# Optimization experiments

Measured on AMD Instinct MI355X. Metric: run time of the kernel, lower is better.

Reference implementation:

```python
import jax, jax.numpy as jnp
import numpy as np

N = 512          # num_atoms (sqrt of number of pairwise edges)
H = 512          # h_nf / in_edge_nf
T_STEPS = 100    # recon.total_time
K_RANK = 3       # coord_dims / low-rank k
POWER_STEPS = 10


def setup_inputs() -> dict:
    key = jax.random.key(0)
    ks = jax.random.split(key, 6)
    s = 1.0 / np.sqrt(H)
    return {
        "gnn_edge_out": jax.random.normal(ks[0], (N * N, H), jnp.float32),
        "W1": jax.random.normal(ks[1], (H, H), jnp.float32) * s,   # edge_mlp1 Linear
        "b1": jnp.zeros((H,), jnp.float32),
        "W2": jax.random.normal(ks[2], (H, 2), jnp.float32) * s,    # edge_mlp2 Linear(h_nf, edge_out_nf=2)
        "b2": jnp.zeros((2,), jnp.float32),
        "noise_x": jax.random.normal(ks[3], (N, K_RANK), jnp.float32),  # randn added to low-rank init
        "u_init": jax.random.normal(ks[4], (N, K_RANK), jnp.float32),   # power-iteration random starts
    }


def reference(gnn_edge_out, W1, b1, W2, b2, noise_x, u_init):
    # ---- DistWeightLayer ----
    h = jax.nn.relu(gnn_edge_out @ W1 + b1)          # edge_mlp1 (MLP, 1 layer)
    emb = jnp.sum(h)[None]                           # sum over dims (0,1), unsqueeze -> (1,)
    e = jax.nn.softplus(h @ W2 + b2)                 # (N*N, 2) softplus(edge_mlp2)
    D_init = e[:, 0].reshape(N, N) * (1.0 - jnp.eye(N, dtype=e.dtype))
    W = e[:, 1].reshape(N, N)

    # ---- dist_to_gram ----
    D = D_init
    D_row = jnp.mean(D, axis=0)                      # (N,)
    D_col = jnp.mean(D, axis=1, keepdims=True)       # (N,1)
    D_mean = jnp.mean(D)
    B = -0.5 * (D - D_row - D_col + D_mean)

    # ---- low_rank_approx_power (k=3, deflation) ----
    A_lr = B
    us = []
    for i in range(K_RANK):
        u = u_init[:, i:i + 1]                       # (N,1)
        for _ in range(POWER_STEPS):
            u = u / jnp.maximum(jnp.linalg.norm(u), 1e-3)  # F.normalize eps=0.001
            u = A_lr @ u
        eig_sq = jnp.sum(u * u)
        u = u * (eig_sq + 0.01) ** 0.25              # u / pow(eig_sq+0.01, -0.25)
        us.append(u)
        A_lr = A_lr - u @ u.T
    X = jnp.concatenate(us, axis=1) + noise_x        # (N,3)

    # ---- 100-step distance-geometry descent (step_func) ----
    def U_fn(Xc):
        diff = Xc[:, None, :] - Xc[None, :, :]       # (N,N,3)
        Dx = jnp.sqrt(jnp.sum(diff * diff, axis=-1) + 0.01)  # tsg_eps
        return jnp.sum(W * jnp.square(D_init - Dx))

    def step(Xc, t):
        g = jax.grad(U_fn)(Xc)
        dX = -0.1 * g                                # tsg_eps1
        speed = jnp.sqrt(jnp.sum(dX * dX, axis=-1, keepdims=True) + 0.001)  # tsg_eps2
        alpha_t = 0.1 + (5.0 - 0.1) * (T_STEPS - t) / T_STEPS
        scale = alpha_t * jnp.tanh(speed / alpha_t) / speed
        return Xc + dX * scale, None

    X_pred, _ = jax.lax.scan(step, X, jnp.arange(T_STEPS, dtype=X.dtype))
    return (D_init, W, emb, X_pred)
```

## Files before the change

kernel.cpp:

```cpp
#include <hip/hip_runtime.h>
#include <hip/hip_bf16.h>
#include <math.h>

#define NN 512
#define ROWS (NN * NN)
#define HH 512

#define NB 16
#define NT 512
#define RPB 32

#define WS_EMB   0
#define WS_COLP  4096
#define WS_U0    (WS_COLP + 32*512)
#define WS_U1    (WS_U0 + 512)
#define WS_X0    (WS_U1 + 512)
#define WS_X1    (WS_X0 + 2048)
#define WS_W1T   (WS_X1 + 2048)
#define WS_BAR   (WS_W1T + 131072)

typedef __attribute__((ext_vector_type(8))) short bf16x8;
typedef __attribute__((ext_vector_type(4))) float f32x4;

#define AGENT __HIP_MEMORY_SCOPE_AGENT

__device__ __forceinline__ short f2bf(float f) {
    union { float f; unsigned u; } v; v.f = f;
    unsigned r = v.u + 0x7fffu + ((v.u >> 16) & 1u);
    return (short)(r >> 16);
}

__device__ __forceinline__ unsigned pack_bf2(float lo, float hi) {
    return __builtin_amdgcn_perm(__float_as_uint(hi), __float_as_uint(lo),
                                 0x07060302u);
}

__device__ __forceinline__ float softplus_f(float x) {
    return fmaxf(x, 0.0f) + log1pf(expf(-fabsf(x)));
}

__device__ __forceinline__ unsigned long long pk64(float a, float b) {
    return ((unsigned long long)__float_as_uint(b) << 32) |
           (unsigned long long)__float_as_uint(a);
}

__global__ void w1t_prep(const float* __restrict__ W1, short* __restrict__ W1T)
{
    __shared__ float tile[32][33];
    const int bx = blockIdx.x & 15;
    const int by = blockIdx.x >> 4;
    const int tx = threadIdx.x & 31;
    const int ty = threadIdx.x >> 5;
    const int n0 = bx * 32, k0 = by * 32;
    #pragma unroll
    for (int i = 0; i < 4; i++)
        tile[ty + i * 8][tx] = W1[(size_t)(k0 + ty + i * 8) * HH + n0 + tx];
    __syncthreads();
    #pragma unroll
    for (int i = 0; i < 4; i++)
        W1T[(size_t)(n0 + ty + i * 8) * HH + k0 + tx] = f2bf(tile[tx][ty + i * 8]);
}

__global__ __launch_bounds__(512, 4) void fused_mlp(
    const float* __restrict__ A, const short* __restrict__ W1T,
    const float* __restrict__ b1, const float* __restrict__ W2,
    const float* __restrict__ b2, float* __restrict__ outD,
    float* __restrict__ outW, float* __restrict__ embpart)
{
    __shared__ short As[2][64 * 72];
    __shared__ float sp0[8][64], sp1[8][64];
    __shared__ float semb[8];

    const int tid = threadIdx.x;
    const int lane = tid & 63;
    const int wc = tid >> 6;
    const int l15 = lane & 15;
    const int l4 = lane >> 4;
    const int row0 = blockIdx.x * 64;

    f32x4 acc[4][4];
    #pragma unroll
    for (int m = 0; m < 4; m++)
        #pragma unroll
        for (int n = 0; n < 4; n++) {
            f32x4 z = {0.0f, 0.0f, 0.0f, 0.0f};
            acc[m][n] = z;
        }

    const int sr = tid >> 3;
    const int sk8 = (tid & 7) * 8;
    const float* agp = A + (size_t)(row0 + sr) * HH + sk8;

    {
        float4 a0 = *(const float4*)agp;
        float4 a1 = *(const float4*)(agp + 4);
        uint4 w = {pack_bf2(a0.x, a0.y), pack_bf2(a0.z, a0.w),
                   pack_bf2(a1.x, a1.y), pack_bf2(a1.z, a1.w)};
        *(uint4*)&As[0][sr * 72 + sk8] = w;
    }
    __syncthreads();

    int cur = 0;
    #pragma unroll 1
    for (int s = 0; s < 8; s++) {
        const int k0 = s * 64;
        float4 pv0, pv1;
        if (s < 7) {
            pv0 = *(const float4*)(agp + k0 + 64);
            pv1 = *(const float4*)(agp + k0 + 68);
        }
        for (int kc = 0; kc < 2; kc++) {
            const int kb = k0 + kc * 32;
            bf16x8 bfr[4], af[4];
            #pragma unroll
            for (int n = 0; n < 4; n++) {
                int col = wc * 64 + n * 16 + l15;
                bfr[n] = *(const bf16x8*)(W1T + (size_t)col * HH + kb + l4 * 8);
            }
            #pragma unroll
            for (int m = 0; m < 4; m++)
                af[m] = *(const bf16x8*)&As[cur][(m * 16 + l15) * 72 + kc * 32 + l4 * 8];
            #pragma unroll
            for (int m = 0; m < 4; m++)
                #pragma unroll
                for (int n = 0; n < 4; n++)
                    acc[m][n] = __builtin_amdgcn_mfma_f32_16x16x32_bf16(
                        af[m], bfr[n], acc[m][n], 0, 0, 0);
        }
        if (s < 7) {
            uint4 w = {pack_bf2(pv0.x, pv0.y), pack_bf2(pv0.z, pv0.w),
                       pack_bf2(pv1.x, pv1.y), pack_bf2(pv1.z, pv1.w)};
            *(uint4*)&As[cur ^ 1][sr * 72 + sk8] = w;
        }
        __syncthreads();
        cur ^= 1;
    }

    float b1c[4], w20[4], w21[4];
    #pragma unroll
    for (int n = 0; n < 4; n++) {
        int col = wc * 64 + n * 16 + l15;
        b1c[n] = b1[col];
        w20[n] = W2[col * 2 + 0];
        w21[n] = W2[col * 2 + 1];
    }
    float embl = 0.0f;
    #pragma unroll
    for (int m = 0; m < 4; m++) {
        #pragma unroll
        for (int j = 0; j < 4; j++) {
            float s0 = 0.0f, s1 = 0.0f;
            #pragma unroll
            for (int n = 0; n < 4; n++) {
                float h = fmaxf(acc[m][n][j] + b1c[n], 0.0f);
                s0 = fmaf(h, w20[n], s0);
                s1 = fmaf(h, w21[n], s1);
                embl += h;
            }
            #pragma unroll
            for (int st = 1; st < 16; st <<= 1) {
                s0 += __shfl_xor(s0, st);
                s1 += __shfl_xor(s1, st);
            }
            if (l15 == 0) {
                int row = m * 16 + l4 * 4 + j;
                sp0[wc][row] = s0;
                sp1[wc][row] = s1;
            }
        }
    }
    #pragma unroll
    for (int st = 1; st < 64; st <<= 1) embl += __shfl_xor(embl, st);
    if (lane == 0) semb[wc] = embl;
    __syncthreads();
    if (tid < 64) {
        int gr = row0 + tid;
        float p0 = b2[0], p1 = b2[1];
        #pragma unroll
        for (int w = 0; w < 8; w++) { p0 += sp0[w][tid]; p1 += sp1[w][tid]; }
        int di = gr >> 9, dj = gr & 511;
        outD[gr] = (di == dj) ? 0.0f : softplus_f(p0);
        outW[gr] = softplus_f(p1);
    }
    if (tid == 0) {
        float e = 0.0f;
        #pragma unroll
        for (int w = 0; w < 8; w++) e += semb[w];
        embpart[blockIdx.x] = e;
    }
}

__device__ __forceinline__ void gbar(int* cnt, int target)
{
    __syncthreads();
    if (threadIdx.x == 0)
        __hip_atomic_fetch_add(cnt, 1, __ATOMIC_RELAXED, AGENT);
    if (threadIdx.x < 64) {
        while (__hip_atomic_load(cnt, __ATOMIC_RELAXED, AGENT) < target)
            __builtin_amdgcn_s_sleep(1);
    }
    __syncthreads();
}

__device__ __forceinline__ void block_sum5(float* v, float (*red)[8], int tid) {
    #pragma unroll
    for (int s = 1; s < 64; s <<= 1)
        #pragma unroll
        for (int q = 0; q < 5; q++) v[q] += __shfl_xor(v[q], s);
    if ((tid & 63) == 0)
        #pragma unroll
        for (int q = 0; q < 5; q++) red[q][tid >> 6] = v[q];
    __syncthreads();
    #pragma unroll
    for (int q = 0; q < 5; q++) {
        float r = 0.0f;
        #pragma unroll
        for (int i = 0; i < 8; i++) r += red[q][i];
        v[q] = r;
    }
    __syncthreads();
}

__device__ __forceinline__ float block_sum1(float v, float (*red)[8], int tid) {
    #pragma unroll
    for (int s = 1; s < 64; s <<= 1) v += __shfl_xor(v, s);
    if ((tid & 63) == 0) red[0][tid >> 6] = v;
    __syncthreads();
    float r = 0.0f;
    #pragma unroll
    for (int i = 0; i < 8; i++) r += red[0][i];
    __syncthreads();
    return r;
}

__global__ __launch_bounds__(512, 1) void coop_post(
    const float* __restrict__ Dg, const float* __restrict__ Wg,
    const float* __restrict__ noise, const float* __restrict__ uinit,
    float* __restrict__ outE, float* __restrict__ outX,
    float* __restrict__ ws)
{
    __shared__ float Dl[RPB][516];
    __shared__ float S1[RPB][516];
    __shared__ float Xl[512][4];
    __shared__ float ul[512];
    __shared__ float upl[3][512];
    __shared__ float cm[512];
    __shared__ float rm[RPB];
    __shared__ float red5[5][8];

    const int tid = threadIdx.x;
    const int bid = blockIdx.x;
    const int r0 = bid * RPB;

    float* embpart = ws + WS_EMB;
    float* colpart = ws + WS_COLP;
    float* ubuf0   = ws + WS_U0;
    float* ubuf1   = ws + WS_U1;
    float* Xg0     = ws + WS_X0;
    float* Xg1     = ws + WS_X1;
    int* cnt       = (int*)(ws + WS_BAR);
    int bg = 0;

    for (int idx = tid; idx < RPB * 512; idx += NT) {
        int r = idx >> 9, c = idx & 511;
        Dl[r][c] = Dg[(size_t)(r0 + r) * NN + c];
    }
    __syncthreads();
    const int mr = tid >> 4;
    const int ml = tid & 15;
    {
        float s = 0.0f;
        for (int j = ml; j < 512; j += 16) s += Dl[mr][j];
        #pragma unroll
        for (int st = 1; st < 16; st <<= 1) s += __shfl_xor(s, st);
        if (ml == 0) rm[mr] = s * (1.0f / 512.0f);
    }
    {
        float s = 0.0f;
        #pragma unroll
        for (int r = 0; r < RPB; r++) s += Dl[r][tid];
        __hip_atomic_store(&colpart[bid * 512 + tid], s, __ATOMIC_RELAXED, AGENT);
    }
    gbar(cnt, NB * ++bg);

    {
        float s = 0.0f;
        #pragma unroll
        for (int p = 0; p < NB; p++)
            s += __hip_atomic_load(&colpart[p * 512 + tid], __ATOMIC_RELAXED, AGENT);
        cm[tid] = s * (1.0f / 512.0f);
    }
    if (bid == 0) {
        float s = 0.0f;
        for (int i = tid; i < ROWS / 64; i += NT) s += embpart[i];
        s = block_sum1(s, red5, tid);
        if (tid == 0) outE[0] = s;
    }
    __syncthreads();
    float Dmean = block_sum1(cm[tid], red5, tid) * (1.0f / 512.0f);

    int cur = 0;
    #pragma unroll 1
    for (int rank = 0; rank < 3; rank++) {
        #pragma unroll 1
        for (int step = 0; step < 10; step++) {
            if (step == 0) {
                ul[tid] = uinit[tid * 3 + rank];
            } else {
                const float* ub = cur ? ubuf1 : ubuf0;
                ul[tid] = __hip_atomic_load(&ub[tid], __ATOMIC_RELAXED, AGENT);
            }
            __syncthreads();
            float u = ul[tid];
            float v[5];
            v[0] = u * u;
            v[1] = u;
            v[2] = cm[tid] * u;
            v[3] = (rank > 0) ? upl[0][tid] * u : 0.0f;
            v[4] = (rank > 1) ? upl[1][tid] * u : 0.0f;
            block_sum5(v, red5, tid);
            float inv = 1.0f / fmaxf(sqrtf(v[0]), 0.001f);
            float S = v[1] * inv, dr = v[2] * inv;
            float d0s = v[3] * inv, d1s = v[4] * inv;
            float a = 0.0f;
            for (int j = ml; j < 512; j += 16) a = fmaf(Dl[mr][j], ul[j], a);
            #pragma unroll
            for (int st = 1; st < 16; st <<= 1) a += __shfl_xor(a, st);
            if (ml == 0) {
                float bvv = -0.5f * (a * inv - dr - rm[mr] * S + Dmean * S);
                if (rank > 0) bvv -= d0s * upl[0][r0 + mr];
                if (rank > 1) bvv -= d1s * upl[1][r0 + mr];
                float* ubn = cur ? ubuf0 : ubuf1;
                __hip_atomic_store(&ubn[r0 + mr], bvv, __ATOMIC_RELAXED, AGENT);
            }
            gbar(cnt, NB * ++bg);
            cur ^= 1;
        }
        {
            const float* ub = cur ? ubuf1 : ubuf0;
            float u = __hip_atomic_load(&ub[tid], __ATOMIC_RELAXED, AGENT);
            float eig2 = block_sum1(u * u, red5, tid);
            float scl = sqrtf(sqrtf(eig2 + 0.01f));
            upl[rank][tid] = u * scl;
            Xl[tid][rank] = fmaf(u, scl, noise[tid * 3 + rank]);
            if (rank == 0) Xl[tid][3] = 0.0f;
            __syncthreads();
        }
    }

    for (int idx = tid; idx < RPB * 512; idx += NT) {
        int r = idx >> 9, j = idx & 511;
        int gr = r0 + r;
        float wr = Wg[(size_t)gr * NN + j];
        float wc = Wg[(size_t)j * NN + gr];
        float dc = Dg[(size_t)j * NN + gr];
        float d  = Dl[r][j];
        S1[r][j] = wr + wc;
        Dl[r][j] = fmaf(wr, d, wc * dc);
    }
    __syncthreads();

    unsigned long long* X064 = (unsigned long long*)Xg0;
    unsigned long long* X164 = (unsigned long long*)Xg1;
    int par = 0;
    #pragma unroll 1
    for (int t = 0; t < 100; t++) {
        float xr0 = Xl[r0 + mr][0], xr1 = Xl[r0 + mr][1], xr2 = Xl[r0 + mr][2];
        float g0 = 0, g1 = 0, g2 = 0;
        for (int j = ml; j < 512; j += 16) {
            float dx0 = xr0 - Xl[j][0];
            float dx1 = xr1 - Xl[j][1];
            float dx2 = xr2 - Xl[j][2];
            float d2 = fmaf(dx0, dx0, fmaf(dx1, dx1, fmaf(dx2, dx2, 0.01f)));
            float ri = rsqrtf(d2);
            float coef = fmaf(Dl[mr][j], ri, -S1[mr][j]);
            g0 = fmaf(coef, dx0, g0);
            g1 = fmaf(coef, dx1, g1);
            g2 = fmaf(coef, dx2, g2);
        }
        #pragma unroll
        for (int st = 1; st < 16; st <<= 1) {
            g0 += __shfl_xor(g0, st);
            g1 += __shfl_xor(g1, st);
            g2 += __shfl_xor(g2, st);
        }
        if (ml == 0) {
            float dX0 = 0.2f * g0, dX1 = 0.2f * g1, dX2 = 0.2f * g2;
            float sp = sqrtf(fmaf(dX0, dX0, fmaf(dX1, dX1, fmaf(dX2, dX2, 0.001f))));
            float alpha = 0.1f + 4.9f * (float)(100 - t) * 0.01f;
            float scal = alpha * tanhf(sp / alpha) / sp;
            float n0 = fmaf(dX0, scal, xr0);
            float n1 = fmaf(dX1, scal, xr1);
            float n2 = fmaf(dX2, scal, xr2);
            int gr = r0 + mr;
            if (t == 99) {
                outX[gr * 3 + 0] = n0;
                outX[gr * 3 + 1] = n1;
                outX[gr * 3 + 2] = n2;
            } else {
                unsigned long long* Xd64 = par ? X164 : X064;
                __hip_atomic_store(&Xd64[gr * 2], pk64(n0, n1),
                                   __ATOMIC_RELAXED, AGENT);
                __hip_atomic_store(&Xd64[gr * 2 + 1], pk64(n2, 0.0f),
                                   __ATOMIC_RELAXED, AGENT);
            }
        }
        if (t == 99) break;
        gbar(cnt, NB * ++bg);
        {
            const unsigned long long* Xs64 = par ? X164 : X064;
            unsigned long long lo =
                __hip_atomic_load(&Xs64[tid * 2], __ATOMIC_RELAXED, AGENT);
            unsigned long long hi =
                __hip_atomic_load(&Xs64[tid * 2 + 1], __ATOMIC_RELAXED, AGENT);
            Xl[tid][0] = __uint_as_float((unsigned)lo);
            Xl[tid][1] = __uint_as_float((unsigned)(lo >> 32));
            Xl[tid][2] = __uint_as_float((unsigned)hi);
            Xl[tid][3] = 0.0f;
        }
        __syncthreads();
        par ^= 1;
    }
}

extern "C" void kernel_launch(void* const* d_in, const int* in_sizes, int n_in,
                              void* d_out, int out_size, void* d_ws, size_t ws_size,
                              hipStream_t stream)
{
    const float* A     = (const float*)d_in[0];
    const float* W1    = (const float*)d_in[1];
    const float* b1    = (const float*)d_in[2];
    const float* W2    = (const float*)d_in[3];
    const float* b2    = (const float*)d_in[4];
    const float* noise = (const float*)d_in[5];
    const float* uinit = (const float*)d_in[6];

    float* out  = (float*)d_out;
    float* outD = out;
    float* outW = out + ROWS;
    float* outE = out + 2 * ROWS;
    float* outX = out + 2 * ROWS + 1;
    float* ws   = (float*)d_ws;
    short* W1T  = (short*)(ws + WS_W1T);

    (void)hipMemsetAsync((char*)d_ws + (size_t)WS_BAR * sizeof(float), 0,
                         512 * sizeof(int), stream);

    hipLaunchKernelGGL(w1t_prep, dim3(256), dim3(256), 0, stream, W1, W1T);

    hipLaunchKernelGGL(fused_mlp, dim3(ROWS / 64), dim3(512), 0, stream,
                       A, W1T, b1, W2, b2, outD, outW, ws + WS_EMB);

    const float* Dg  = outD;
    const float* Wgc = outW;
    void* args[] = { (void*)&Dg, (void*)&Wgc, (void*)&noise, (void*)&uinit,
                     (void*)&outE, (void*)&outX, (void*)&ws };
    (void)hipLaunchCooperativeKernel((const void*)coop_post, dim3(NB), dim3(NT),
                                     args, 0, stream);
}
```

Baseline: 953.4 us.

## Prefetch W1T fragments into registers and use per-block flag barrier

The GEMM loop now double-buffers the B-operand (W1T) fragments in registers, issuing global loads for the next k-chunk while MFMAs run on the current one, so global load latency is hidden. Separately, the grid barrier is changed from a single shared atomic counter to per-block generation flags that each block writes and the first NB threads poll, avoiding contention on one atomic. This costs more registers in the GEMM and relies on the flags being zeroed in the workspace beforehand.

```diff
diff --git a/kernel.cpp b/kernel.cpp
--- a/kernel.cpp
+++ b/kernel.cpp
@@ -91,12 +91,25 @@
     const int sk8 = (tid & 7) * 8;
     const float* agp = A + (size_t)(row0 + sr) * HH + sk8;
 
+    const short* bP[4];
+    #pragma unroll
+    for (int n = 0; n < 4; n++) {
+        int col = wc * 64 + n * 16 + l15;
+        bP[n] = W1T + (size_t)col * HH + l4 * 8;
+    }
+
     {
         float4 a0 = *(const float4*)agp;
         float4 a1 = *(const float4*)(agp + 4);
         uint4 w = {pack_bf2(a0.x, a0.y), pack_bf2(a0.z, a0.w),
                    pack_bf2(a1.x, a1.y), pack_bf2(a1.z, a1.w)};
         *(uint4*)&As[0][sr * 72 + sk8] = w;
+    }
+    bf16x8 bfrA[4], bfrB[4];
+    #pragma unroll
+    for (int n = 0; n < 4; n++) {
+        bfrA[n] = *(const bf16x8*)(bP[n]);
+        bfrB[n] = *(const bf16x8*)(bP[n] + 32);
     }
     __syncthreads();
 
@@ -109,25 +122,39 @@
             pv0 = *(const float4*)(agp + k0 + 64);
             pv1 = *(const float4*)(agp + k0 + 68);
         }
-        for (int kc = 0; kc < 2; kc++) {
-            const int kb = k0 + kc * 32;
-            bf16x8 bfr[4], af[4];
-            #pragma unroll
-            for (int n = 0; n < 4; n++) {
-                int col = wc * 64 + n * 16 + l15;
-                bfr[n] = *(const bf16x8*)(W1T + (size_t)col * HH + kb + l4 * 8);
-            }
+        {
+            bf16x8 af[4];
             #pragma unroll
             for (int m = 0; m < 4; m++)
-                af[m] = *(const bf16x8*)&As[cur][(m * 16 + l15) * 72 + kc * 32 + l4 * 8];
+                af[m] = *(const bf16x8*)&As[cur][(m * 16 + l15) * 72 + l4 * 8];
             #pragma unroll
             for (int m = 0; m < 4; m++)
                 #pragma unroll
                 for (int n = 0; n < 4; n++)
                     acc[m][n] = __builtin_amdgcn_mfma_f32_16x16x32_bf16(
-                        af[m], bfr[n], acc[m][n], 0, 0, 0);
+                        af[m], bfrA[n], acc[m][n], 0, 0, 0);
         }
         if (s < 7) {
+            #pragma unroll
+            for (int n = 0; n < 4; n++)
+                bfrA[n] = *(const bf16x8*)(bP[n] + k0 + 64);
+        }
+        {
+            bf16x8 af[4];
+            #pragma unroll
+            for (int m = 0; m < 4; m++)
+                af[m] = *(const bf16x8*)&As[cur][(m * 16 + l15) * 72 + 32 + l4 * 8];
+            #pragma unroll
+            for (int m = 0; m < 4; m++)
+                #pragma unroll
+                for (int n = 0; n < 4; n++)
+                    acc[m][n] = __builtin_amdgcn_mfma_f32_16x16x32_bf16(
+                        af[m], bfrB[n], acc[m][n], 0, 0, 0);
+        }
+        if (s < 7) {
+            #pragma unroll
+            for (int n = 0; n < 4; n++)
+                bfrB[n] = *(const bf16x8*)(bP[n] + k0 + 96);
             uint4 w = {pack_bf2(pv0.x, pv0.y), pack_bf2(pv0.z, pv0.w),
                        pack_bf2(pv1.x, pv1.y), pack_bf2(pv1.z, pv1.w)};
             *(uint4*)&As[cur ^ 1][sr * 72 + sk8] = w;
@@ -190,13 +217,13 @@
     }
 }
 
-__device__ __forceinline__ void gbar(int* cnt, int target)
+__device__ __forceinline__ void gbar(int* flags, int gen)
 {
     __syncthreads();
     if (threadIdx.x == 0)
-        __hip_atomic_fetch_add(cnt, 1, __ATOMIC_RELAXED, AGENT);
-    if (threadIdx.x < 64) {
-        while (__hip_atomic_load(cnt, __ATOMIC_RELAXED, AGENT) < target)
+        __hip_atomic_store(&flags[blockIdx.x], gen, __ATOMIC_RELAXED, AGENT);
+    if (threadIdx.x < NB) {
+        while (__hip_atomic_load(&flags[threadIdx.x], __ATOMIC_RELAXED, AGENT) < gen)
             __builtin_amdgcn_s_sleep(1);
     }
     __syncthreads();
@@ -258,7 +285,7 @@
     float* ubuf1   = ws + WS_U1;
     float* Xg0     = ws + WS_X0;
     float* Xg1     = ws + WS_X1;
-    int* cnt       = (int*)(ws + WS_BAR);
+    int* flags     = (int*)(ws + WS_BAR);
     int bg = 0;
 
     for (int idx = tid; idx < RPB * 512; idx += NT) {
@@ -281,7 +308,7 @@
         for (int r = 0; r < RPB; r++) s += Dl[r][tid];
         __hip_atomic_store(&colpart[bid * 512 + tid], s, __ATOMIC_RELAXED, AGENT);
     }
-    gbar(cnt, NB * ++bg);
+    gbar(flags, ++bg);
 
     {
         float s = 0.0f;
@@ -333,7 +360,7 @@
                 float* ubn = cur ? ubuf0 : ubuf1;
                 __hip_atomic_store(&ubn[r0 + mr], bvv, __ATOMIC_RELAXED, AGENT);
             }
-            gbar(cnt, NB * ++bg);
+            gbar(flags, ++bg);
             cur ^= 1;
         }
         {
@@ -406,7 +433,7 @@
             }
         }
         if (t == 99) break;
-        gbar(cnt, NB * ++bg);
+        gbar(flags, ++bg);
         {
             const unsigned long long* Xs64 = par ? X164 : X064;
             unsigned long long lo =
```

New measurement: 1.011 ms. 1.06x slower.

## Pre-swizzle W1 into MFMA fragment order and shrink K-stage to 32

Applied to the files above, without the earlier changes.

The prep kernel now writes W1 as bf16 in the exact per-lane MFMA B-fragment order, so each wave's B loads become fully contiguous 16-byte-per-lane reads instead of strided row accesses. The main GEMM loop moves from 64-wide K stages to 32-wide stages with a smaller LDS A buffer, doubling the number of barriers but cutting LDS use and per-stage register pressure. The aim is to reduce global/L2 traffic inefficiency on the weight operand, at the cost of more synchronization iterations and less prefetch lookahead per stage.

```diff
diff --git a/kernel.cpp b/kernel.cpp
--- a/kernel.cpp
+++ b/kernel.cpp
@@ -16,8 +16,8 @@
 #define WS_U1    (WS_U0 + 512)
 #define WS_X0    (WS_U1 + 512)
 #define WS_X1    (WS_X0 + 2048)
-#define WS_W1T   (WS_X1 + 2048)
-#define WS_BAR   (WS_W1T + 131072)
+#define WS_W1F   (WS_X1 + 2048)
+#define WS_BAR   (WS_W1F + 131072)
 
 typedef __attribute__((ext_vector_type(8))) short bf16x8;
 typedef __attribute__((ext_vector_type(4))) float f32x4;
@@ -44,30 +44,29 @@
            (unsigned long long)__float_as_uint(a);
 }
 
-__global__ void w1t_prep(const float* __restrict__ W1, short* __restrict__ W1T)
+__global__ void w1f_prep(const float* __restrict__ W1, short* __restrict__ W1F)
 {
-    __shared__ float tile[32][33];
-    const int bx = blockIdx.x & 15;
-    const int by = blockIdx.x >> 4;
-    const int tx = threadIdx.x & 31;
-    const int ty = threadIdx.x >> 5;
-    const int n0 = bx * 32, k0 = by * 32;
-    #pragma unroll
-    for (int i = 0; i < 4; i++)
-        tile[ty + i * 8][tx] = W1[(size_t)(k0 + ty + i * 8) * HH + n0 + tx];
-    __syncthreads();
-    #pragma unroll
-    for (int i = 0; i < 4; i++)
-        W1T[(size_t)(n0 + ty + i * 8) * HH + k0 + tx] = f2bf(tile[tx][ty + i * 8]);
+    const int c = blockIdx.x * 256 + threadIdx.x;
+    const int lane = c & 63;
+    const int g = c >> 6;
+    const int colg = g & 31;
+    const int kc = g >> 5;
+    const int col = colg * 16 + (lane & 15);
+    const int kb = kc * 32 + (lane >> 4) * 8;
+    bf16x8 w;
+    #pragma unroll
+    for (int j = 0; j < 8; j++)
+        w[j] = f2bf(W1[(size_t)(kb + j) * HH + col]);
+    *(bf16x8*)(W1F + (size_t)c * 8) = w;
 }
 
 __global__ __launch_bounds__(512, 4) void fused_mlp(
-    const float* __restrict__ A, const short* __restrict__ W1T,
+    const float* __restrict__ A, const short* __restrict__ W1F,
     const float* __restrict__ b1, const float* __restrict__ W2,
     const float* __restrict__ b2, float* __restrict__ outD,
     float* __restrict__ outW, float* __restrict__ embpart)
 {
-    __shared__ short As[2][64 * 72];
+    __shared__ short As[2][64 * 40];
     __shared__ float sp0[8][64], sp1[8][64];
     __shared__ float semb[8];
 
@@ -88,49 +87,41 @@
         }
 
     const int sr = tid >> 3;
-    const int sk8 = (tid & 7) * 8;
-    const float* agp = A + (size_t)(row0 + sr) * HH + sk8;
+    const int sk4 = (tid & 7) * 4;
+    const float* agp = A + (size_t)(row0 + sr) * HH + sk4;
+
+    const short* bfp = W1F + ((size_t)(wc * 4) * 64 + lane) * 8;
 
     {
         float4 a0 = *(const float4*)agp;
-        float4 a1 = *(const float4*)(agp + 4);
-        uint4 w = {pack_bf2(a0.x, a0.y), pack_bf2(a0.z, a0.w),
-                   pack_bf2(a1.x, a1.y), pack_bf2(a1.z, a1.w)};
-        *(uint4*)&As[0][sr * 72 + sk8] = w;
+        uint2 w = {pack_bf2(a0.x, a0.y), pack_bf2(a0.z, a0.w)};
+        *(uint2*)&As[0][sr * 40 + sk4] = w;
     }
     __syncthreads();
 
     int cur = 0;
     #pragma unroll 1
-    for (int s = 0; s < 8; s++) {
-        const int k0 = s * 64;
-        float4 pv0, pv1;
-        if (s < 7) {
-            pv0 = *(const float4*)(agp + k0 + 64);
-            pv1 = *(const float4*)(agp + k0 + 68);
-        }
-        for (int kc = 0; kc < 2; kc++) {
-            const int kb = k0 + kc * 32;
-            bf16x8 bfr[4], af[4];
+    for (int s = 0; s < 16; s++) {
+        const int k0 = s * 32;
+        bf16x8 bfr[4];
+        #pragma unroll
+        for (int n = 0; n < 4; n++)
+            bfr[n] = *(const bf16x8*)(bfp + s * 16384 + n * 512);
+        float4 pv;
+        if (s < 15) pv = *(const float4*)(agp + k0 + 32);
+        bf16x8 af[4];
+        #pragma unroll
+        for (int m = 0; m < 4; m++)
+            af[m] = *(const bf16x8*)&As[cur][(m * 16 + l15) * 40 + l4 * 8];
+        #pragma unroll
+        for (int m = 0; m < 4; m++)
             #pragma unroll
-            for (int n = 0; n < 4; n++) {
-                int col = wc * 64 + n * 16 + l15;
-                bfr[n] = *(const bf16x8*)(W1T + (size_t)col * HH + kb + l4 * 8);
-            }
-            #pragma unroll
-            for (int m = 0; m < 4; m++)
-                af[m] = *(const bf16x8*)&As[cur][(m * 16 + l15) * 72 + kc * 32 + l4 * 8];
-            #pragma unroll
-            for (int m = 0; m < 4; m++)
-                #pragma unroll
-                for (int n = 0; n < 4; n++)
-                    acc[m][n] = __builtin_amdgcn_mfma_f32_16x16x32_bf16(
-                        af[m], bfr[n], acc[m][n], 0, 0, 0);
-        }
-        if (s < 7) {
-            uint4 w = {pack_bf2(pv0.x, pv0.y), pack_bf2(pv0.z, pv0.w),
-                       pack_bf2(pv1.x, pv1.y), pack_bf2(pv1.z, pv1.w)};
-            *(uint4*)&As[cur ^ 1][sr * 72 + sk8] = w;
+            for (int n = 0; n < 4; n++)
+                acc[m][n] = __builtin_amdgcn_mfma_f32_16x16x32_bf16(
+                    af[m], bfr[n], acc[m][n], 0, 0, 0);
+        if (s < 15) {
+            uint2 w = {pack_bf2(pv.x, pv.y), pack_bf2(pv.z, pv.w)};
+            *(uint2*)&As[cur ^ 1][sr * 40 + sk4] = w;
         }
         __syncthreads();
         cur ^= 1;
@@ -441,15 +432,15 @@
     float* outE = out + 2 * ROWS;
     float* outX = out + 2 * ROWS + 1;
     float* ws   = (float*)d_ws;
-    short* W1T  = (short*)(ws + WS_W1T);
+    short* W1F  = (short*)(ws + WS_W1F);
 
     (void)hipMemsetAsync((char*)d_ws + (size_t)WS_BAR * sizeof(float), 0,
                          512 * sizeof(int), stream);
 
-    hipLaunchKernelGGL(w1t_prep, dim3(256), dim3(256), 0, stream, W1, W1T);
+    hipLaunchKernelGGL(w1f_prep, dim3(128), dim3(256), 0, stream, W1, W1F);
 
     hipLaunchKernelGGL(fused_mlp, dim3(ROWS / 64), dim3(512), 0, stream,
-                       A, W1T, b1, W2, b2, outD, outW, ws + WS_EMB);
+                       A, W1F, b1, W2, b2, outD, outW, ws + WS_EMB);
 
     const float* Dg  = outD;
     const float* Wgc = outW;
```

Measured after the change: 863.7 us. -9.4%, faster.
